# Kernel tuning notes

Measured on AMD Instinct MI355X. Metric: run time of the kernel, lower is better.

The kernel has to match this reference:

```python
import jax, jax.numpy as jnp
import numpy as np
import math

B, T, C = 4, 2048, 1024
N_HEAD = 16


def setup_inputs() -> dict:
    key = jax.random.key(0)
    k1, k2, k3 = jax.random.split(key, 3)
    x = jax.random.normal(k1, (B, T, C), dtype=jnp.float32)
    W_attn = jax.random.normal(k2, (C, 3 * C), dtype=jnp.float32) * (1.0 / math.sqrt(C))
    b_attn = jnp.zeros((3 * C,), dtype=jnp.float32)
    W_proj = jax.random.normal(k3, (C, C), dtype=jnp.float32) * (1.0 / math.sqrt(C))
    b_proj = jnp.zeros((C,), dtype=jnp.float32)
    return {"x": x, "W_attn": W_attn, "b_attn": b_attn, "W_proj": W_proj, "b_proj": b_proj}


def reference(x, W_attn, b_attn, W_proj, b_proj):
    b, t, c = x.shape
    hs = c // N_HEAD  # head size
    qkv = x @ W_attn + b_attn  # [B,T,3C]
    q, k, v = jnp.split(qkv, 3, axis=-1)
    # [B,T,C] -> [B,H,T,hs]
    q = q.reshape(b, t, N_HEAD, hs).transpose(0, 2, 1, 3)
    k = k.reshape(b, t, N_HEAD, hs).transpose(0, 2, 1, 3)
    v = v.reshape(b, t, N_HEAD, hs).transpose(0, 2, 1, 3)
    att = jnp.einsum('bhqd,bhkd->bhqk', q, k) / math.sqrt(hs)  # [B,H,T,T]
    causal = jnp.tril(jnp.ones((t, t), dtype=bool))
    att = jnp.where(causal[None, None, :, :], att, -jnp.inf)
    att = jax.nn.softmax(att, axis=-1)
    y = jnp.einsum('bhqk,bhkd->bhqd', att, v)  # [B,H,T,hs]
    y = y.transpose(0, 2, 1, 3).reshape(b, t, c)
    return y @ W_proj + b_proj
```

## Files before the change

kernel.cpp:

```cpp
#include <hip/hip_runtime.h>


typedef __bf16 bf16_t;
typedef __bf16 bf16x8 __attribute__((ext_vector_type(8)));
typedef __bf16 bf16x4 __attribute__((ext_vector_type(4)));
typedef float  f32x4  __attribute__((ext_vector_type(4)));

#define MFMA16(a, b, c) __builtin_amdgcn_mfma_f32_16x16x32_bf16((a), (b), (c), 0, 0, 0)

static __device__ __forceinline__ void gld_lds16(const bf16_t* g, void* l) {
  __builtin_amdgcn_global_load_lds(
      (const __attribute__((address_space(1))) void*)(const void*)g,
      (__attribute__((address_space(3))) void*)l, 16, 0, 0);
}

static __device__ __forceinline__ bf16x8 ldv8(const void* p) {
  return *reinterpret_cast<const bf16x8*>(p);
}

static __device__ __forceinline__ float exp2_hw(float x) {
  float r;
  asm("v_exp_f32 %0, %1" : "=v"(r) : "v"(x));
  return r;
}

__global__ __launch_bounds__(256) void cvt_f32_bf16(const float* __restrict__ in,
                                                    bf16_t* __restrict__ out, int n4) {
  int i = blockIdx.x * 256 + threadIdx.x;
  if (i < n4) {
    float4 v = reinterpret_cast<const float4*>(in)[i];
    bf16x4 o;
    o[0] = (bf16_t)v.x; o[1] = (bf16_t)v.y; o[2] = (bf16_t)v.z; o[3] = (bf16_t)v.w;
    reinterpret_cast<bf16x4*>(out)[i] = o;
  }
}

__global__ __launch_bounds__(256) void transpose_cvt(const float* __restrict__ in,
                                                     bf16_t* __restrict__ out,
                                                     int Kd, int Nd) {
  __shared__ float tile[32][33];
  int tx = threadIdx.x, ty = threadIdx.y;
  int n0 = blockIdx.x * 32, k0 = blockIdx.y * 32;
#pragma unroll
  for (int i = 0; i < 4; ++i)
    tile[ty + i * 8][tx] = in[(size_t)(k0 + ty + i * 8) * Nd + (n0 + tx)];
  __syncthreads();
#pragma unroll
  for (int i = 0; i < 4; ++i)
    out[(size_t)(n0 + ty + i * 8) * Kd + (k0 + tx)] = (bf16_t)tile[tx][ty + i * 8];
}

template <int MODE, int KD>
__global__ __launch_bounds__(256) void gemm_bf16(
    const bf16_t* __restrict__ A, const bf16_t* __restrict__ Bt,
    const float* __restrict__ bias, int M, int N,
    bf16_t* __restrict__ Qo, bf16_t* __restrict__ Ko, bf16_t* __restrict__ Vt,
    float* __restrict__ Co) {
  __shared__ alignas(16) char lds[32768];

  const int tid = threadIdx.x;
  const int wave = tid >> 6, lane = tid & 63;
  const int wm = wave >> 1, wn = wave & 1;
  const int l16 = lane & 15, kb = lane >> 4;
  const int r7 = l16 & 7;

  const int nbx = gridDim.x;
  const int lb = blockIdx.y * nbx + blockIdx.x;
  const int c = lb & 7;
  const int ii = lb >> 3;
  const int rPer = gridDim.y >> 3;
  const int tmt = c * rPer + (ii % rPer);
  const int tnt = ii / rPer;
  const int tm0 = tmt * 128, tn0 = tnt * 128;

  const int srow = wave * 8 + (lane >> 3);
  const int sp = lane & 7;

  unsigned aOff[2][4], bOff[2][4];
#pragma unroll
  for (int kc = 0; kc < 2; ++kc)
#pragma unroll
    for (int i = 0; i < 4; ++i) {
      const int rowA = wm * 64 + i * 16 + l16;
      const int rowB = wn * 64 + i * 16 + l16;
      const int slot = (kc * 4 + kb) ^ r7;
      aOff[kc][i] = rowA * 128 + slot * 16;
      bOff[kc][i] = 16384 + rowB * 128 + slot * 16;
    }

  const bf16_t* aR = A + (size_t)(tm0 + srow) * KD + sp * 8;
  const bf16_t* bR = Bt + (size_t)(tn0 + srow) * KD + sp * 8;
  const int schx = ((sp ^ (srow & 7)) - sp) * 8;

  f32x4 acc[4][4] = {};

  for (int k0 = 0; k0 < KD; k0 += 64) {
    __syncthreads();
#pragma unroll
    for (int inst = 0; inst < 4; ++inst) {
      gld_lds16(aR + (size_t)(inst * 32) * KD + k0 + schx,
                &lds[inst * 4096 + wave * 1024]);
      gld_lds16(bR + (size_t)(inst * 32) * KD + k0 + schx,
                &lds[16384 + inst * 4096 + wave * 1024]);
    }
    __syncthreads();
#pragma unroll
    for (int kc = 0; kc < 2; ++kc) {
      bf16x8 af[4], bfr[4];
#pragma unroll
      for (int mi = 0; mi < 4; ++mi) af[mi] = ldv8(&lds[aOff[kc][mi]]);
#pragma unroll
      for (int ni = 0; ni < 4; ++ni) bfr[ni] = ldv8(&lds[bOff[kc][ni]]);
#pragma unroll
      for (int mi = 0; mi < 4; ++mi)
#pragma unroll
        for (int ni = 0; ni < 4; ++ni)
          acc[mi][ni] = MFMA16(af[mi], bfr[ni], acc[mi][ni]);
    }
  }

  if constexpr (MODE == 0) {
    const int which = tn0 >> 10;
    const int bb = tm0 >> 11;
    const int t0 = (tm0 & 2047) + wm * 64 + kb * 4;
    const int hn0 = (tn0 & 1023) + wn * 64;
    const int hh = bb * 16 + (hn0 >> 6);

    if (which == 2) {
#pragma unroll
      for (int ni = 0; ni < 4; ++ni) {
        const int d = ni * 16 + l16;
        const float bv = bias[2048 + hn0 + d];
        bf16_t* p = Vt + ((size_t)hh * 64 + d) * 2048;
#pragma unroll
        for (int mi = 0; mi < 4; ++mi) {
          bf16x4 v4;
#pragma unroll
          for (int j = 0; j < 4; ++j) v4[j] = (bf16_t)(acc[mi][ni][j] + bv);
          *reinterpret_cast<bf16x4*>(&p[t0 + mi * 16]) = v4;
        }
      }
    } else {
      bf16_t* dst = which ? Ko : Qo;
      const float scl = which ? 1.0f : 0.18033688011112042f;
#pragma unroll
      for (int ni = 0; ni < 4; ++ni) {
        const int d = ni * 16 + l16;
        const float bv = bias[which * 1024 + hn0 + d];
        bf16_t* p = dst + (size_t)hh * 131072 + d;
#pragma unroll
        for (int mi = 0; mi < 4; ++mi)
#pragma unroll
          for (int j = 0; j < 4; ++j)
            p[(size_t)(t0 + mi * 16 + j) * 64] = (bf16_t)((acc[mi][ni][j] + bv) * scl);
      }
    }
  } else {
#pragma unroll
    for (int ni = 0; ni < 4; ++ni) {
      const int n = tn0 + wn * 64 + ni * 16 + l16;
      const float bv = bias[n];
#pragma unroll
      for (int mi = 0; mi < 4; ++mi) {
#pragma unroll
        for (int j = 0; j < 4; ++j) {
          const int m = tm0 + wm * 64 + mi * 16 + kb * 4 + j;
          Co[(size_t)m * N + n] = acc[mi][ni][j] + bv;
        }
      }
    }
  }
}

__global__ __launch_bounds__(256) void attn_fwd(const bf16_t* __restrict__ Qg,
                                                const bf16_t* __restrict__ Kg,
                                                const bf16_t* __restrict__ Vtg,
                                                bf16_t* __restrict__ Yg) {
  __shared__ alignas(16) char lds[40960];

  const int tid = threadIdx.x;
  const int wave = tid >> 6, lane = tid & 63;
  const int l16 = lane & 15, kb = lane >> 4;
  const int l8 = l16 & 7;
  const float NEG_INF = -__builtin_inff();

  const int n = blockIdx.x;
  const int bh = (n & 7) * 8 + ((n >> 3) & 7);
  const int qt = 31 - (n >> 6);
  const size_t base = (size_t)bh * (2048 * 64);
  const int b = bh >> 4, h = bh & 15;

  const int srow = tid >> 3;
  const int schunk = (tid & 7) ^ (srow & 7);
  const bf16_t* Ksrc = Kg + base + (size_t)srow * 64 + schunk * 8;
  const bf16_t* Vsrc = Vtg + base + (size_t)srow * 2048 + schunk * 8;

  auto stageK = [&](int buf, int kv0) {
    char* kd = lds + buf * 8192 + wave * 1024;
    const bf16_t* ks = Ksrc + (size_t)kv0 * 64;
    gld_lds16(ks, kd);
    gld_lds16(ks + 2048, kd + 4096);
  };
  auto stageV = [&](int buf, int kv0) {
    char* vd = lds + 16384 + buf * 8192 + wave * 1024;
    const bf16_t* vs = Vsrc + kv0;
    gld_lds16(vs, vd);
    gld_lds16(vs + 65536, vd + 4096);
  };

  const int q0 = qt * 64 + wave * 16;
  const int q = q0 + l16;
  const int trips = qt + 1;

  const bf16x8 qf0 = ldv8(Qg + base + (size_t)q * 64 + kb * 8);
  const bf16x8 qf1 = ldv8(Qg + base + (size_t)q * 64 + 32 + kb * 8);

  f32x4 o[4] = {};
  float l_r = 0.f;

  char* Pw = lds + 32768 + wave * 2048;
  const unsigned rb0 = l16 * 128 + ((kb ^ l8) * 16);
  const unsigned rb1 = l16 * 128 + (((4 + kb) ^ l8) * 16);

  stageK(0, 0);
  stageV(0, 0);
  asm volatile("s_waitcnt vmcnt(0)" ::: "memory");
  __builtin_amdgcn_s_barrier();
  __builtin_amdgcn_sched_barrier(0);

  int cur = 0;
  for (int t = 0; t < trips; ++t) {
    const int kv0 = t * 64;
    const bool more = (t + 1 < trips);
    if (more) {
      stageK(cur ^ 1, kv0 + 64);
      stageV(cur ^ 1, kv0 + 64);
    }

    const char* k0p = lds + cur * 8192 + rb0;
    const char* k1p = lds + cur * 8192 + rb1;
    const char* v0p = lds + 16384 + cur * 8192 + rb0;
    const char* v1p = lds + 16384 + cur * 8192 + rb1;

    bf16x8 kf[8];
#pragma unroll
    for (int i = 0; i < 4; ++i) {
      kf[i * 2 + 0] = ldv8(k0p + i * 2048);
      kf[i * 2 + 1] = ldv8(k1p + i * 2048);
    }

    f32x4 s[4];
#pragma unroll
    for (int i = 0; i < 4; ++i) s[i] = f32x4{-16.f, -16.f, -16.f, -16.f};
    __builtin_amdgcn_s_setprio(1);
#pragma unroll
    for (int i = 0; i < 4; ++i) {
      s[i] = MFMA16(kf[i * 2 + 0], qf0, s[i]);
      s[i] = MFMA16(kf[i * 2 + 1], qf1, s[i]);
    }
    __builtin_amdgcn_s_setprio(0);

    bf16x8 vf[8];
#pragma unroll
    for (int i = 0; i < 4; ++i) {
      vf[i * 2 + 0] = ldv8(v0p + i * 2048);
      vf[i * 2 + 1] = ldv8(v1p + i * 2048);
    }

    if (t == qt) {
#pragma unroll
      for (int i = 0; i < 4; ++i)
#pragma unroll
        for (int j = 0; j < 4; ++j)
          if (kv0 + i * 16 + kb * 4 + j > q) s[i][j] = NEG_INF;
    }

    float ss = 0.f;
    bf16x4 pw[4];
#pragma unroll
    for (int i = 0; i < 4; ++i)
#pragma unroll
      for (int j = 0; j < 4; ++j) {
        const float p = exp2_hw(s[i][j]);
        ss += p;
        pw[i][j] = (bf16_t)p;
      }
    l_r += ss;

#pragma unroll
    for (int i = 0; i < 4; ++i) {
      const int phys = (i * 2 + (kb >> 1)) ^ l8;
      *reinterpret_cast<bf16x4*>(Pw + l16 * 128 + phys * 16 + (kb & 1) * 8) = pw[i];
    }
    const bf16x8 pb0 = ldv8(Pw + l16 * 128 + ((kb ^ l8) * 16));
    const bf16x8 pb1 = ldv8(Pw + l16 * 128 + (((4 + kb) ^ l8) * 16));

    __builtin_amdgcn_s_setprio(1);
#pragma unroll
    for (int i = 0; i < 4; ++i) {
      o[i] = MFMA16(vf[i * 2 + 0], pb0, o[i]);
      o[i] = MFMA16(vf[i * 2 + 1], pb1, o[i]);
    }
    __builtin_amdgcn_s_setprio(0);

    asm volatile("s_waitcnt vmcnt(0)" ::: "memory");
    __builtin_amdgcn_s_barrier();
    __builtin_amdgcn_sched_barrier(0);
    cur ^= 1;
  }

  float lt = l_r + __shfl_xor(l_r, 16);
  lt += __shfl_xor(lt, 32);
  const float inv = 1.0f / lt;
  bf16_t* yrow = Yg + ((size_t)(b * 2048 + q)) * 1024 + h * 64;
#pragma unroll
  for (int i = 0; i < 4; ++i) {
    bf16x4 yv;
    yv[0] = (bf16_t)(o[i][0] * inv);
    yv[1] = (bf16_t)(o[i][1] * inv);
    yv[2] = (bf16_t)(o[i][2] * inv);
    yv[3] = (bf16_t)(o[i][3] * inv);
    *reinterpret_cast<bf16x4*>(yrow + i * 16 + kb * 4) = yv;
  }
}

extern "C" void kernel_launch(void* const* d_in, const int* in_sizes, int n_in,
                              void* d_out, int out_size, void* d_ws, size_t ws_size,
                              hipStream_t stream) {
  const float* x = (const float*)d_in[0];
  const float* W_attn = (const float*)d_in[1];
  const float* b_attn = (const float*)d_in[2];
  const float* W_proj = (const float*)d_in[3];
  const float* b_proj = (const float*)d_in[4];
  float* out = (float*)d_out;

  char* ws = (char*)d_ws;
  bf16_t* xb  = (bf16_t*)(ws + 0);
  bf16_t* WaT = (bf16_t*)(ws + 16777216);
  bf16_t* WpT = (bf16_t*)(ws + 23068672);
  bf16_t* Qb  = (bf16_t*)(ws + 25165824);
  bf16_t* Kb  = (bf16_t*)(ws + 41943040);
  bf16_t* Vt  = (bf16_t*)(ws + 58720256);
  bf16_t* Yb  = (bf16_t*)(ws + 75497472);

  cvt_f32_bf16<<<8192, 256, 0, stream>>>(x, xb, 8192 * 1024 / 4);
  transpose_cvt<<<dim3(96, 32), dim3(32, 8), 0, stream>>>(W_attn, WaT, 1024, 3072);
  transpose_cvt<<<dim3(32, 32), dim3(32, 8), 0, stream>>>(W_proj, WpT, 1024, 1024);

  gemm_bf16<0, 1024><<<dim3(24, 64), 256, 0, stream>>>(xb, WaT, b_attn, 8192, 3072,
                                                       Qb, Kb, Vt, nullptr);

  attn_fwd<<<2048, 256, 0, stream>>>(Qb, Kb, Vt, Yb);

  gemm_bf16<1, 1024><<<dim3(8, 64), 256, 0, stream>>>(Yb, WpT, b_proj, 8192, 1024,
                                                      nullptr, nullptr, nullptr, out);
}
```

Baseline: 157.8 us.

## Load K/V fragments directly from global in attention and fuse prep kernels

The attention kernel drops the double-buffered global-to-LDS staging of K and V tiles and its per-iteration barriers. Each wave now loads its MFMA fragments straight from global memory, keeping LDS only for the P transpose, which shrinks LDS use and may raise occupancy. It also merges the x conversion and the two weight transpose-converts into one launch to cut launch overhead. The risk is that the four waves of a block now each fetch the same K/V data separately with no prefetch, so global load latency is exposed on every iteration.

```diff
diff --git a/kernel.cpp b/kernel.cpp
--- a/kernel.cpp
+++ b/kernel.cpp
@@ -24,30 +24,37 @@
   return r;
 }
 
-__global__ __launch_bounds__(256) void cvt_f32_bf16(const float* __restrict__ in,
-                                                    bf16_t* __restrict__ out, int n4) {
-  int i = blockIdx.x * 256 + threadIdx.x;
-  if (i < n4) {
-    float4 v = reinterpret_cast<const float4*>(in)[i];
+__global__ __launch_bounds__(256) void prep_fused(
+    const float* __restrict__ x, bf16_t* __restrict__ xb,
+    const float* __restrict__ Wa, bf16_t* __restrict__ WaT,
+    const float* __restrict__ Wp, bf16_t* __restrict__ WpT) {
+  __shared__ float tile[32][33];
+  const int bid = blockIdx.x;
+  const int tid = threadIdx.x;
+
+  if (bid < 8192) {
+    const int i = bid * 256 + tid;
+    float4 v = reinterpret_cast<const float4*>(x)[i];
     bf16x4 o;
     o[0] = (bf16_t)v.x; o[1] = (bf16_t)v.y; o[2] = (bf16_t)v.z; o[3] = (bf16_t)v.w;
-    reinterpret_cast<bf16x4*>(out)[i] = o;
-  }
-}
-
-__global__ __launch_bounds__(256) void transpose_cvt(const float* __restrict__ in,
-                                                     bf16_t* __restrict__ out,
-                                                     int Kd, int Nd) {
-  __shared__ float tile[32][33];
-  int tx = threadIdx.x, ty = threadIdx.y;
-  int n0 = blockIdx.x * 32, k0 = blockIdx.y * 32;
+    reinterpret_cast<bf16x4*>(xb)[i] = o;
+    return;
+  }
+  const bool isA = bid < 11264;
+  const int tb = isA ? (bid - 8192) : (bid - 11264);
+  const int Nd = isA ? 3072 : 1024;
+  const int nbx = isA ? 96 : 32;
+  const float* in = isA ? Wa : Wp;
+  bf16_t* out = isA ? WaT : WpT;
+  const int n0 = (tb % nbx) * 32, k0 = (tb / nbx) * 32;
+  const int tx = tid & 31, ty = tid >> 5;
 #pragma unroll
   for (int i = 0; i < 4; ++i)
     tile[ty + i * 8][tx] = in[(size_t)(k0 + ty + i * 8) * Nd + (n0 + tx)];
   __syncthreads();
 #pragma unroll
   for (int i = 0; i < 4; ++i)
-    out[(size_t)(n0 + ty + i * 8) * Kd + (k0 + tx)] = (bf16_t)tile[tx][ty + i * 8];
+    out[(size_t)(n0 + ty + i * 8) * 1024 + (k0 + tx)] = (bf16_t)tile[tx][ty + i * 8];
 }
 
 template <int MODE, int KD>
@@ -176,7 +183,7 @@
                                                 const bf16_t* __restrict__ Kg,
                                                 const bf16_t* __restrict__ Vtg,
                                                 bf16_t* __restrict__ Yg) {
-  __shared__ alignas(16) char lds[40960];
+  __shared__ alignas(16) char lds[8192];
 
   const int tid = threadIdx.x;
   const int wave = tid >> 6, lane = tid & 63;
@@ -190,24 +197,6 @@
   const size_t base = (size_t)bh * (2048 * 64);
   const int b = bh >> 4, h = bh & 15;
 
-  const int srow = tid >> 3;
-  const int schunk = (tid & 7) ^ (srow & 7);
-  const bf16_t* Ksrc = Kg + base + (size_t)srow * 64 + schunk * 8;
-  const bf16_t* Vsrc = Vtg + base + (size_t)srow * 2048 + schunk * 8;
-
-  auto stageK = [&](int buf, int kv0) {
-    char* kd = lds + buf * 8192 + wave * 1024;
-    const bf16_t* ks = Ksrc + (size_t)kv0 * 64;
-    gld_lds16(ks, kd);
-    gld_lds16(ks + 2048, kd + 4096);
-  };
-  auto stageV = [&](int buf, int kv0) {
-    char* vd = lds + 16384 + buf * 8192 + wave * 1024;
-    const bf16_t* vs = Vsrc + kv0;
-    gld_lds16(vs, vd);
-    gld_lds16(vs + 65536, vd + 4096);
-  };
-
   const int q0 = qt * 64 + wave * 16;
   const int q = q0 + l16;
   const int trips = qt + 1;
@@ -218,35 +207,28 @@
   f32x4 o[4] = {};
   float l_r = 0.f;
 
-  char* Pw = lds + 32768 + wave * 2048;
-  const unsigned rb0 = l16 * 128 + ((kb ^ l8) * 16);
-  const unsigned rb1 = l16 * 128 + (((4 + kb) ^ l8) * 16);
-
-  stageK(0, 0);
-  stageV(0, 0);
-  asm volatile("s_waitcnt vmcnt(0)" ::: "memory");
-  __builtin_amdgcn_s_barrier();
-  __builtin_amdgcn_sched_barrier(0);
-
-  int cur = 0;
+  char* Pw = lds + wave * 2048;
+  unsigned pwOff[4];
+#pragma unroll
+  for (int i = 0; i < 4; ++i) {
+    const int phys = (i * 2 + (kb >> 1)) ^ l8;
+    pwOff[i] = l16 * 128 + phys * 16 + (kb & 1) * 8;
+  }
+  const unsigned pr0 = l16 * 128 + ((kb ^ l8) * 16);
+  const unsigned pr1 = l16 * 128 + (((4 + kb) ^ l8) * 16);
+
+  const bf16_t* Kl = Kg + base + (size_t)l16 * 64 + kb * 8;
+  const bf16_t* Vl = Vtg + base + (size_t)l16 * 2048 + kb * 8;
+
   for (int t = 0; t < trips; ++t) {
     const int kv0 = t * 64;
-    const bool more = (t + 1 < trips);
-    if (more) {
-      stageK(cur ^ 1, kv0 + 64);
-      stageV(cur ^ 1, kv0 + 64);
-    }
-
-    const char* k0p = lds + cur * 8192 + rb0;
-    const char* k1p = lds + cur * 8192 + rb1;
-    const char* v0p = lds + 16384 + cur * 8192 + rb0;
-    const char* v1p = lds + 16384 + cur * 8192 + rb1;
 
     bf16x8 kf[8];
 #pragma unroll
     for (int i = 0; i < 4; ++i) {
-      kf[i * 2 + 0] = ldv8(k0p + i * 2048);
-      kf[i * 2 + 1] = ldv8(k1p + i * 2048);
+      const bf16_t* kr = Kl + (size_t)(kv0 + i * 16) * 64;
+      kf[i * 2 + 0] = ldv8(kr);
+      kf[i * 2 + 1] = ldv8(kr + 32);
     }
 
     f32x4 s[4];
@@ -263,8 +245,9 @@
     bf16x8 vf[8];
 #pragma unroll
     for (int i = 0; i < 4; ++i) {
-      vf[i * 2 + 0] = ldv8(v0p + i * 2048);
-      vf[i * 2 + 1] = ldv8(v1p + i * 2048);
+      const bf16_t* vr = Vl + (size_t)(i * 16) * 2048 + kv0;
+      vf[i * 2 + 0] = ldv8(vr);
+      vf[i * 2 + 1] = ldv8(vr + 32);
     }
 
     if (t == qt) {
@@ -288,12 +271,10 @@
     l_r += ss;
 
 #pragma unroll
-    for (int i = 0; i < 4; ++i) {
-      const int phys = (i * 2 + (kb >> 1)) ^ l8;
-      *reinterpret_cast<bf16x4*>(Pw + l16 * 128 + phys * 16 + (kb & 1) * 8) = pw[i];
-    }
-    const bf16x8 pb0 = ldv8(Pw + l16 * 128 + ((kb ^ l8) * 16));
-    const bf16x8 pb1 = ldv8(Pw + l16 * 128 + (((4 + kb) ^ l8) * 16));
+    for (int i = 0; i < 4; ++i)
+      *reinterpret_cast<bf16x4*>(Pw + pwOff[i]) = pw[i];
+    const bf16x8 pb0 = ldv8(Pw + pr0);
+    const bf16x8 pb1 = ldv8(Pw + pr1);
 
     __builtin_amdgcn_s_setprio(1);
 #pragma unroll
@@ -302,11 +283,6 @@
       o[i] = MFMA16(vf[i * 2 + 1], pb1, o[i]);
     }
     __builtin_amdgcn_s_setprio(0);
-
-    asm volatile("s_waitcnt vmcnt(0)" ::: "memory");
-    __builtin_amdgcn_s_barrier();
-    __builtin_amdgcn_sched_barrier(0);
-    cur ^= 1;
   }
 
   float lt = l_r + __shfl_xor(l_r, 16);
@@ -343,9 +319,7 @@
   bf16_t* Vt  = (bf16_t*)(ws + 58720256);
   bf16_t* Yb  = (bf16_t*)(ws + 75497472);
 
-  cvt_f32_bf16<<<8192, 256, 0, stream>>>(x, xb, 8192 * 1024 / 4);
-  transpose_cvt<<<dim3(96, 32), dim3(32, 8), 0, stream>>>(W_attn, WaT, 1024, 3072);
-  transpose_cvt<<<dim3(32, 32), dim3(32, 8), 0, stream>>>(W_proj, WpT, 1024, 1024);
+  prep_fused<<<12288, 256, 0, stream>>>(x, xb, W_attn, WaT, W_proj, WpT);
 
   gemm_bf16<0, 1024><<<dim3(24, 64), 256, 0, stream>>>(xb, WaT, b_attn, 8192, 3072,
                                                        Qb, Kb, Vt, nullptr);
```

New measurement: 336.2 us. +113.0%, slower.
